# Optimization experiments

Hardware: AMD Instinct MI355X
Metric: run time of the kernel (lower is better)

The kernel has to match this reference:

```python
import jax, jax.numpy as jnp
import numpy as np

INPUT_DIM = 512
QUERY_DIM = 512
NUM_HEAD = 8
HEAD_DIM = INPUT_DIM // NUM_HEAD
SQRT_INPUT_DIM = INPUT_DIM ** 0.5
ELU_CLIP = 15.0  # elu_clip: elu followed by clamp to [-15, 15] (keeps exp finite)


def elu_clip(x):
    return jnp.clip(jax.nn.elu(x), -ELU_CLIP, ELU_CLIP)


def setup_inputs() -> dict:
    key = jax.random.key(0)
    k1, k2, k3, k4, k5, k6, k7 = jax.random.split(key, 7)
    B, S, Q = 8, 4096, 32
    inputs = jax.random.normal(k1, (B, S, INPUT_DIM), dtype=jnp.float32)
    queries = jax.random.normal(k2, (B, Q, QUERY_DIM), dtype=jnp.float32)
    masks = (jax.random.uniform(k3, (B, S)) > 0.1).astype(jnp.float32)
    # torch Linear params: weight [out, in], bias [out]
    lim_kv = 1.0 / np.sqrt(INPUT_DIM)
    Wkv = jax.random.uniform(k4, (2 * INPUT_DIM, INPUT_DIM), minval=-lim_kv, maxval=lim_kv, dtype=jnp.float32)
    bkv = jax.random.uniform(k5, (2 * INPUT_DIM,), minval=-lim_kv, maxval=lim_kv, dtype=jnp.float32)
    lim_q = 1.0 / np.sqrt(QUERY_DIM)
    Wq = jax.random.uniform(k6, (INPUT_DIM, QUERY_DIM), minval=-lim_q, maxval=lim_q, dtype=jnp.float32)
    bq = jax.random.uniform(k7, (INPUT_DIM,), minval=-lim_q, maxval=lim_q, dtype=jnp.float32)
    return {"inputs": inputs, "queries": queries, "masks": masks,
            "Wkv": Wkv, "bkv": bkv, "Wq": Wq, "bq": bq}


def reference(inputs, queries, masks, Wkv, bkv, Wq, bq):
    B, S, _ = inputs.shape
    Q = queries.shape[1]
    # k, v projections: [B,S,2I] -> [B,S,2,H,D]; index 0 along dim 2 is k, 1 is v
    kv = (inputs @ Wkv.T + bkv).reshape(B, S, 2, NUM_HEAD, HEAD_DIM)
    k, v = kv[:, :, 0], kv[:, :, 1]          # [B,S,H,D]
    q = (queries @ Wq.T + bq).reshape(B, Q, NUM_HEAD, HEAD_DIM)  # [B,Q,H,D]
    # scores: broadcast dot-product per head -> [B,Q,S,H]
    u = jnp.einsum('bqhd,bshd->bqsh', q, k)
    exp_u = jnp.exp(elu_clip(u / SQRT_INPUT_DIM))
    exp_u = exp_u * masks[:, None, :, None]
    attention = exp_u / jnp.sum(exp_u, axis=2, keepdims=True)
    # weighted sum over sequence -> [B,Q,H,D] -> [B,Q,I]
    attend = jnp.einsum('bqsh,bshd->bqhd', attention, v).reshape(B, Q, INPUT_DIM)
    return attend
```

## Files before the change

kernel.cpp:

```cpp
#include <hip/hip_runtime.h>
#include <hip/hip_bf16.h>


typedef float f32x4 __attribute__((ext_vector_type(4)));
typedef short s16x8 __attribute__((ext_vector_type(8)));

__device__ __forceinline__ unsigned short f2bf(float f) {
  union { __hip_bfloat16 h; unsigned short u; } cv;
  cv.h = __float2bfloat16(f);
  return cv.u;
}
__device__ __forceinline__ float bf2f(unsigned short u) {
  union { unsigned short u; __hip_bfloat16 h; } cv;
  cv.u = u;
  return __bfloat162float(cv.h);
}
__device__ __forceinline__ float tofl(float v) { return v; }
__device__ __forceinline__ float tofl(__hip_bfloat16 v) { return __bfloat162float(v); }

__device__ __forceinline__ f32x4 mfma16(s16x8 a, s16x8 b, f32x4 c) {
  return __builtin_amdgcn_mfma_f32_16x16x32_bf16(a, b, c, 0, 0, 0);
}

__device__ __forceinline__ int detect_fp32(const unsigned short* __restrict__ in16) {
  unsigned short v = in16[2 * (threadIdx.x & 63)];
  int e = (v >> 7) & 0xFF;
  unsigned long long m = __ballot(e >= 100 && e <= 130);
  return __popcll(m) < 48 ? 1 : 0;
}

__device__ __forceinline__ void gload_lds16(const void* g, void* s) {
  __builtin_amdgcn_global_load_lds(
      (const __attribute__((address_space(1))) unsigned int*)(g),
      (__attribute__((address_space(3))) unsigned int*)(s), 16, 0, 0);
}

__device__ __forceinline__ unsigned short* stg(unsigned short* buf, int r, int u) {
  return buf + r * 64 + ((u ^ (r & 7)) << 3);
}
__device__ __forceinline__ const unsigned short* stgc(const unsigned short* buf, int r, int u) {
  return buf + r * 64 + ((u ^ (r & 7)) << 3);
}
__device__ __forceinline__ int sw_idx(int r, int c) {
  return r * 128 + ((((c >> 3) ^ (r & 7)) << 3) | (c & 7));
}

template <typename T>
__device__ __forceinline__ s16x8 load_frag8(const T* p);
template <>
__device__ __forceinline__ s16x8 load_frag8<float>(const float* p) {
  const float4* q = reinterpret_cast<const float4*>(p);
  float4 a = q[0], b = q[1];
  union { unsigned short u[8]; s16x8 w; } t;
  t.u[0] = f2bf(a.x); t.u[1] = f2bf(a.y); t.u[2] = f2bf(a.z); t.u[3] = f2bf(a.w);
  t.u[4] = f2bf(b.x); t.u[5] = f2bf(b.y); t.u[6] = f2bf(b.z); t.u[7] = f2bf(b.w);
  return t.w;
}
template <>
__device__ __forceinline__ s16x8 load_frag8<__hip_bfloat16>(const __hip_bfloat16* p) {
  return *reinterpret_cast<const s16x8*>(p);
}

template <typename T> struct RegChunk;
template <> struct RegChunk<float> {
  float4 v[4];
  __device__ __forceinline__ void load(const float* p) {
    const float4* q = reinterpret_cast<const float4*>(p);
    v[0] = q[0]; v[1] = q[1]; v[2] = q[2]; v[3] = q[3];
  }
  __device__ __forceinline__ void store(unsigned short* d) {
    union { unsigned short u[16]; s16x8 w[2]; } t;
    const float* f = reinterpret_cast<const float*>(v);
#pragma unroll
    for (int i = 0; i < 16; ++i) t.u[i] = f2bf(f[i]);
    reinterpret_cast<s16x8*>(d)[0] = t.w[0];
    reinterpret_cast<s16x8*>(d)[1] = t.w[1];
  }
  __device__ __forceinline__ void store2(unsigned short* d0, unsigned short* d1) {
    union { unsigned short u[16]; s16x8 w[2]; } t;
    const float* f = reinterpret_cast<const float*>(v);
#pragma unroll
    for (int i = 0; i < 16; ++i) t.u[i] = f2bf(f[i]);
    *reinterpret_cast<s16x8*>(d0) = t.w[0];
    *reinterpret_cast<s16x8*>(d1) = t.w[1];
  }
};
template <> struct RegChunk<__hip_bfloat16> {
  s16x8 v[2];
  __device__ __forceinline__ void load(const __hip_bfloat16* p) {
    const s16x8* q = reinterpret_cast<const s16x8*>(p);
    v[0] = q[0]; v[1] = q[1];
  }
  __device__ __forceinline__ void store(unsigned short* d) {
    reinterpret_cast<s16x8*>(d)[0] = v[0];
    reinterpret_cast<s16x8*>(d)[1] = v[1];
  }
  __device__ __forceinline__ void store2(unsigned short* d0, unsigned short* d1) {
    *reinterpret_cast<s16x8*>(d0) = v[0];
    *reinterpret_cast<s16x8*>(d1) = v[1];
  }
};


#define CINP 0
#define CQ   16777216
#define CWKV 16908288
#define CWQ  17432576
#define CBKV 17694720
#define CBQ  17695744
#define CTOT 17696256

__global__ __launch_bounds__(256) void k_conv(const void* inputs, const void* queries,
                                              const void* Wkv, const void* Wq,
                                              const void* bkv, const void* bq,
                                              unsigned short* __restrict__ dst) {
  const int fp32 = detect_fp32((const unsigned short*)inputs);
  if (!fp32) return;
  const int bid = blockIdx.x, tid = threadIdx.x;
  if (bid < 2048) {
    size_t u = (size_t)bid * 1024 + tid;
#pragma unroll
    for (int k = 0; k < 4; ++k, u += 256) {
      size_t e = u * 8;
      s16x8 v = load_frag8<float>((const float*)inputs + e);
      *reinterpret_cast<s16x8*>(dst + e) = v;
    }
  } else {
    size_t i8 = (size_t)(bid - 2048) * 256 + tid;
    for (; i8 < 114880; i8 += (size_t)72 * 256) {
      size_t e = CQ + i8 * 8;
      const void* src;
      size_t off;
      if (e < CWKV) { src = queries; off = e - CQ; }
      else if (e < CWQ) { src = Wkv; off = e - CWKV; }
      else if (e < CBKV) { src = Wq; off = e - CWQ; }
      else if (e < CBQ) { src = bkv; off = e - CBKV; }
      else { src = bq; off = e - CBQ; }
      s16x8 v = load_frag8<float>((const float*)src + off);
      *reinterpret_cast<s16x8*>(dst + e) = v;
    }
  }
}

__global__ __launch_bounds__(256) void k_gemm2(const unsigned short* __restrict__ c,
                                               const void* inputs, const void* queries,
                                               const void* Wkv, const void* Wq,
                                               const void* bkv, const void* bq,
                                               unsigned short* __restrict__ kv,
                                               unsigned short* __restrict__ qws) {
  __shared__ unsigned short Ab[128 * 64];
  __shared__ unsigned short Bb[128 * 64];

  const int fp32 = detect_fp32((const unsigned short*)inputs);

  const int bid = blockIdx.x;
  const int t = (bid & 7) * 257 + (bid >> 3);
  const unsigned short *A, *W, *bias;
  unsigned short* dst;
  int dstride, Mt, Nt;
  if (t < 2048) {
    if (fp32) { A = c + CINP; W = c + CWKV; bias = c + CBKV; }
    else {
      A = (const unsigned short*)inputs;
      W = (const unsigned short*)Wkv;
      bias = (const unsigned short*)bkv;
    }
    dst = kv; dstride = 1024; Mt = t >> 3; Nt = t & 7;
  } else {
    const int tq = t - 2048;
    if (fp32) { A = c + CQ; W = c + CWQ; bias = c + CBQ; }
    else {
      A = (const unsigned short*)queries;
      W = (const unsigned short*)Wq;
      bias = (const unsigned short*)bq;
    }
    dst = qws; dstride = 512; Mt = tq >> 2; Nt = tq & 3;
  }

  const int tid = threadIdx.x;
  const int w = tid >> 6, l = tid & 63;
  const int quad = l >> 4, l16 = l & 15;
  const int wr = (w >> 1) * 64, wc = (w & 1) * 64;

  const int lrow = l >> 3;
  const int gsw = (l & 7) ^ lrow;

  const f32x4 zero4 = {0.f, 0.f, 0.f, 0.f};
  f32x4 acc[4][4];
#pragma unroll
  for (int i = 0; i < 4; ++i)
#pragma unroll
    for (int j = 0; j < 4; ++j) acc[i][j] = zero4;

  const size_t arow0 = (size_t)(Mt * 128) * 512;
  const size_t brow0 = (size_t)(Nt * 128) * 512;

#pragma unroll
  for (int k0 = 0; k0 < 512; k0 += 64) {
    __syncthreads();
#pragma unroll
    for (int k = 0; k < 4; ++k) {
      const int row = w * 32 + k * 8 + lrow;
      const int srcc = k0 + gsw * 8;
      gload_lds16(A + arow0 + (size_t)row * 512 + srcc, Ab + (w * 32 + k * 8) * 64);
      gload_lds16(W + brow0 + (size_t)row * 512 + srcc, Bb + (w * 32 + k * 8) * 64);
    }
    __syncthreads();
#pragma unroll
    for (int kk2 = 0; kk2 < 2; ++kk2) {
      s16x8 af[4], bfr[4];
#pragma unroll
      for (int i = 0; i < 4; ++i)
        af[i] = *reinterpret_cast<const s16x8*>(stgc(Ab, wr + i * 16 + l16, kk2 * 4 + quad));
#pragma unroll
      for (int j = 0; j < 4; ++j)
        bfr[j] = *reinterpret_cast<const s16x8*>(stgc(Bb, wc + j * 16 + l16, kk2 * 4 + quad));
#pragma unroll
      for (int i = 0; i < 4; ++i)
#pragma unroll
        for (int j = 0; j < 4; ++j) acc[i][j] = mfma16(af[i], bfr[j], acc[i][j]);
    }
  }

#pragma unroll
  for (int j = 0; j < 4; ++j) {
    float bb = bf2f(bias[Nt * 128 + wc + j * 16 + l16]);
#pragma unroll
    for (int i = 0; i < 4; ++i)
#pragma unroll
      for (int rg = 0; rg < 4; ++rg) {
        int row = Mt * 128 + wr + i * 16 + quad * 4 + rg;
        int col = Nt * 128 + wc + j * 16 + l16;
        dst[(size_t)row * dstride + col] = f2bf(acc[i][j][rg] + bb);
      }
  }
}

template <typename T>
__device__ __forceinline__ void attn_body(const unsigned short* __restrict__ kv,
                                          const unsigned short* __restrict__ qws,
                                          const T* __restrict__ masks,
                                          float* __restrict__ num_part,
                                          float* __restrict__ den_part,
                                          unsigned short* kvb, unsigned short* vtb,
                                          unsigned short* Pb, float* denL) {
  const int stile = blockIdx.x, b = blockIdx.y;
  const int s0 = stile * 128;
  const int tid = threadIdx.x;
  const int w = tid >> 6, l = tid & 63;
  const int quad = l >> 4, l16 = l & 15;
  const int hh = w >> 2, mt = (w >> 1) & 1, sh = w & 1, dh = w & 1;
  const int sr2 = tid >> 2, c0 = (tid & 3) * 32;
  const int rp2 = (tid >> 3) * 2;
  const int cb = (tid & 7) * 16;
  const f32x4 zero4 = {0.f, 0.f, 0.f, 0.f};
  const float scale = 0.044194173824159216f;
  const int bstile = b * 32 + stile;

  const unsigned short* kbase = kv + ((size_t)(b * 4096 + s0 + sr2)) * 1024;
  const unsigned short* vbase0 = kv + ((size_t)(b * 4096 + s0 + rp2)) * 1024 + 512;
  const unsigned short* vbase1 = vbase0 + 1024;

  s16x8 kp0, kp1, kp2, kp3, va0, va1, vb0, vb1;
  auto loadKV = [&](int hpi) {
    const unsigned short* kr = kbase + hpi * 128 + c0;
    kp0 = *reinterpret_cast<const s16x8*>(kr);
    kp1 = *reinterpret_cast<const s16x8*>(kr + 8);
    kp2 = *reinterpret_cast<const s16x8*>(kr + 16);
    kp3 = *reinterpret_cast<const s16x8*>(kr + 24);
    const unsigned short* v0 = vbase0 + hpi * 128 + cb;
    const unsigned short* v1 = vbase1 + hpi * 128 + cb;
    va0 = *reinterpret_cast<const s16x8*>(v0);
    va1 = *reinterpret_cast<const s16x8*>(v0 + 8);
    vb0 = *reinterpret_cast<const s16x8*>(v1);
    vb1 = *reinterpret_cast<const s16x8*>(v1 + 8);
  };
  loadKV(0);

#pragma unroll
  for (int hpi = 0; hpi < 4; ++hpi) {
    *reinterpret_cast<s16x8*>(&kvb[sw_idx(sr2, c0)]) = kp0;
    *reinterpret_cast<s16x8*>(&kvb[sw_idx(sr2, c0 + 8)]) = kp1;
    *reinterpret_cast<s16x8*>(&kvb[sw_idx(sr2, c0 + 16)]) = kp2;
    *reinterpret_cast<s16x8*>(&kvb[sw_idx(sr2, c0 + 24)]) = kp3;
    {
      union { s16x8 w; unsigned short u[8]; } a0, a1, b0, b1;
      a0.w = va0; a1.w = va1; b0.w = vb0; b1.w = vb1;
#pragma unroll
      for (int e = 0; e < 8; ++e) {
        unsigned int p0 = (unsigned int)a0.u[e] | ((unsigned int)b0.u[e] << 16);
        *reinterpret_cast<unsigned int*>(&vtb[sw_idx(cb + e, rp2)]) = p0;
        unsigned int p1 = (unsigned int)a1.u[e] | ((unsigned int)b1.u[e] << 16);
        *reinterpret_cast<unsigned int*>(&vtb[sw_idx(cb + 8 + e, rp2)]) = p1;
      }
    }
    if (hpi < 3) loadKV(hpi + 1);
    __syncthreads();

    {
      f32x4 ua[4];
#pragma unroll
      for (int j = 0; j < 4; ++j) ua[j] = zero4;
#pragma unroll
      for (int kk = 0; kk < 2; ++kk) {
        s16x8 aq = *reinterpret_cast<const s16x8*>(
            &qws[((size_t)(b * 32 + mt * 16 + l16)) * 512 + hpi * 128 + hh * 64 + kk * 32 +
                 quad * 8]);
#pragma unroll
        for (int j = 0; j < 4; ++j) {
          s16x8 bk = *reinterpret_cast<const s16x8*>(
              &kvb[sw_idx(sh * 64 + j * 16 + l16, hh * 64 + kk * 32 + quad * 8)]);
          ua[j] = mfma16(aq, bk, ua[j]);
        }
      }
      float dsum[4] = {0.f, 0.f, 0.f, 0.f};
#pragma unroll
      for (int j = 0; j < 4; ++j) {
        int scol = sh * 64 + j * 16 + l16;
        float mask = tofl(masks[(size_t)b * 4096 + s0 + scol]);
#pragma unroll
        for (int rg = 0; rg < 4; ++rg) {
          int qrow = mt * 16 + quad * 4 + rg;
          float uv = ua[j][rg] * scale;
          float e = uv > 0.f ? uv : (__expf(uv) - 1.f);
          e = fminf(e, 15.f);
          float p = __expf(e) * mask;
          unsigned short pu = f2bf(p);
          Pb[sw_idx(hh * 32 + qrow, scol)] = pu;
          dsum[rg] += bf2f(pu);
        }
      }
#pragma unroll
      for (int rg = 0; rg < 4; ++rg) {
        float s = dsum[rg];
        s += __shfl_xor(s, 1);
        s += __shfl_xor(s, 2);
        s += __shfl_xor(s, 4);
        s += __shfl_xor(s, 8);
        if (l16 == 0) denL[sh * 64 + hh * 32 + mt * 16 + quad * 4 + rg] = s;
      }
    }
    __syncthreads();

    if (tid < 64) {
      int qrow = tid & 31, hd = tid >> 5;
      den_part[((size_t)bstile * 32 + qrow) * 8 + hpi * 2 + hd] =
          denL[hd * 32 + qrow] + denL[64 + hd * 32 + qrow];
    }

    {
      f32x4 na0 = zero4, na1 = zero4;
#pragma unroll
      for (int kk = 0; kk < 4; ++kk) {
        s16x8 ap = *reinterpret_cast<const s16x8*>(
            &Pb[sw_idx(hh * 32 + mt * 16 + l16, kk * 32 + quad * 8)]);
        s16x8 bv0 = *reinterpret_cast<const s16x8*>(
            &vtb[sw_idx(hh * 64 + dh * 32 + l16, kk * 32 + quad * 8)]);
        s16x8 bv1 = *reinterpret_cast<const s16x8*>(
            &vtb[sw_idx(hh * 64 + dh * 32 + 16 + l16, kk * 32 + quad * 8)]);
        na0 = mfma16(ap, bv0, na0);
        na1 = mfma16(ap, bv1, na1);
      }
#pragma unroll
      for (int rg = 0; rg < 4; ++rg) {
        int qrow = mt * 16 + quad * 4 + rg;
        size_t base = ((size_t)bstile * 32 + qrow) * 512 + (hpi * 2 + hh) * 64 + dh * 32;
        num_part[base + l16] = na0[rg];
        num_part[base + 16 + l16] = na1[rg];
      }
    }
    __syncthreads();
  }
}

__global__ __launch_bounds__(512) void k_attn(const unsigned short* __restrict__ kv,
                                              const unsigned short* __restrict__ qws,
                                              const void* masks, float* __restrict__ num_part,
                                              float* __restrict__ den_part,
                                              const unsigned short* __restrict__ det) {
  __shared__ unsigned short kvb[128 * 128];
  __shared__ unsigned short vtb[128 * 128];
  __shared__ unsigned short Pb[64 * 128];
  __shared__ float denL[128];
  if (detect_fp32(det))
    attn_body<float>(kv, qws, (const float*)masks, num_part, den_part, kvb, vtb, Pb, denL);
  else
    attn_body<__hip_bfloat16>(kv, qws, (const __hip_bfloat16*)masks, num_part, den_part,
                              kvb, vtb, Pb, denL);
}

__global__ __launch_bounds__(256) void k_final(const float* __restrict__ num_part,
                                               const float* __restrict__ den_part, void* out,
                                               const unsigned short* __restrict__ det) {
  int i = blockIdx.x * 256 + threadIdx.x;
  int b = i >> 14, qhd = i & 16383;
  int q = (i >> 9) & 31, h = (i >> 6) & 7;
  float sn = 0.f, sd = 0.f;
#pragma unroll 4
  for (int st = 0; st < 32; ++st) {
    sn += num_part[(((size_t)(b * 32 + st)) << 14) + qhd];
    sd += den_part[((size_t)(b * 32 + st) * 32 + q) * 8 + h];
  }
  float v = sn / sd;
  if (detect_fp32(det))
    ((float*)out)[i] = v;
  else
    ((__hip_bfloat16*)out)[i] = __float2bfloat16(v);
}

template <typename T>
__device__ __forceinline__ void qproj_body_fb(const T* __restrict__ queries,
                                              const T* __restrict__ Wq,
                                              const T* __restrict__ bq,
                                              unsigned short* __restrict__ qws,
                                              unsigned short* Abuf, unsigned short* Bbuf) {
  const int Mt = blockIdx.x, Nt = blockIdx.y;
  const int tid = threadIdx.x;
  const int w = tid >> 6, l = tid & 63;
  const int quad = l >> 4, l16 = l & 15;
  const int wr = (w >> 1) * 64, wc = (w & 1) * 64;
  const int r_st = tid >> 1;
  const int kk_st = (tid & 1) * 16;
  const T* Asrc = queries + ((size_t)(Mt * 128 + r_st)) * 512 + kk_st;
  const T* Bsrc = Wq + ((size_t)(Nt * 128 + r_st)) * 512 + kk_st;

  const f32x4 zero4 = {0.f, 0.f, 0.f, 0.f};
  f32x4 acc[4][4];
#pragma unroll
  for (int i = 0; i < 4; ++i)
#pragma unroll
    for (int j = 0; j < 4; ++j) acc[i][j] = zero4;

  RegChunk<T> ra, rb;
  ra.load(Asrc);
  rb.load(Bsrc);
  for (int k0 = 0; k0 < 512; k0 += 32) {
    __syncthreads();
    ra.store(&Abuf[r_st * 32 + kk_st]);
    rb.store(&Bbuf[r_st * 32 + kk_st]);
    if (k0 + 32 < 512) {
      ra.load(Asrc + k0 + 32);
      rb.load(Bsrc + k0 + 32);
    }
    __syncthreads();
    s16x8 af[4], bfr[4];
#pragma unroll
    for (int i = 0; i < 4; ++i)
      af[i] = *reinterpret_cast<const s16x8*>(&Abuf[(wr + i * 16 + l16) * 32 + quad * 8]);
#pragma unroll
    for (int j = 0; j < 4; ++j)
      bfr[j] = *reinterpret_cast<const s16x8*>(&Bbuf[(wc + j * 16 + l16) * 32 + quad * 8]);
#pragma unroll
    for (int i = 0; i < 4; ++i)
#pragma unroll
      for (int j = 0; j < 4; ++j) acc[i][j] = mfma16(af[i], bfr[j], acc[i][j]);
  }
#pragma unroll
  for (int j = 0; j < 4; ++j) {
    float bb = tofl(bq[Nt * 128 + wc + j * 16 + l16]);
#pragma unroll
    for (int i = 0; i < 4; ++i)
#pragma unroll
      for (int rg = 0; rg < 4; ++rg) {
        int row = Mt * 128 + wr + i * 16 + quad * 4 + rg;
        int col = Nt * 128 + wc + j * 16 + l16;
        qws[(size_t)row * 512 + col] = f2bf(acc[i][j][rg] + bb);
      }
  }
}

__global__ __launch_bounds__(256) void k_qproj_fb(const void* queries, const void* Wq,
                                                  const void* bq, unsigned short* qws,
                                                  const unsigned short* __restrict__ det) {
  __shared__ unsigned short Abuf[128 * 32];
  __shared__ unsigned short Bbuf[128 * 32];
  if (detect_fp32(det))
    qproj_body_fb<float>((const float*)queries, (const float*)Wq, (const float*)bq, qws,
                         Abuf, Bbuf);
  else
    qproj_body_fb<__hip_bfloat16>((const __hip_bfloat16*)queries,
                                  (const __hip_bfloat16*)Wq, (const __hip_bfloat16*)bq, qws,
                                  Abuf, Bbuf);
}

template <typename T>
__device__ __forceinline__ void fused_body_fb(
    const T* __restrict__ inputs, const T* __restrict__ masks, const T* __restrict__ Wkv,
    const T* __restrict__ bkv, const unsigned short* __restrict__ qws,
    float* __restrict__ num, float* __restrict__ den, unsigned short* Abuf,
    unsigned short* Bbuf, unsigned short* kvbuf, unsigned short* vbuf,
    unsigned short* Pbuf) {
  const int stile = blockIdx.x;
  const int b = blockIdx.y;
  const int hp = blockIdx.z;
  const int s0 = stile * 128;
  const int tid = threadIdx.x;
  const int w = tid >> 6;
  const int l = tid & 63;
  const int quad = l >> 4;
  const int l16 = l & 15;
  const int which = w >> 2;
  const int wr = ((w >> 1) & 1) * 64;
  const int wc = (w & 1) * 64;

  const f32x4 zero4 = {0.f, 0.f, 0.f, 0.f};
  f32x4 acc[4][4];
#pragma unroll
  for (int i = 0; i < 4; ++i)
#pragma unroll
    for (int j = 0; j < 4; ++j) acc[i][j] = zero4;

  const int sr = tid >> 2;
  const int sc = tid & 3;
  const T* Asrc = inputs + ((size_t)(b * 4096 + s0 + sr)) * 512 + sc * 16;
  const T* BKs = Wkv + ((size_t)(hp * 128 + sr)) * 512 + sc * 16;
  const T* BVs = Wkv + ((size_t)(512 + hp * 128 + sr)) * 512 + sc * 16;
  unsigned short* ad0 = stg(Abuf, sr, sc * 2);
  unsigned short* ad1 = stg(Abuf, sr, sc * 2 + 1);
  unsigned short* bk0 = stg(Bbuf, sr, sc * 2);
  unsigned short* bk1 = stg(Bbuf, sr, sc * 2 + 1);
  unsigned short* bv0 = stg(Bbuf, 128 + sr, sc * 2);
  unsigned short* bv1 = stg(Bbuf, 128 + sr, sc * 2 + 1);

  RegChunk<T> ra0, ra1, rbk, rbv;
  ra0.load(Asrc);
  ra1.load(Asrc + 64);
  rbk.load(BKs);
  rbv.load(BVs);

#pragma unroll
  for (int it2 = 0; it2 < 4; ++it2) {
#pragma unroll
    for (int ph = 0; ph < 2; ++ph) {
      const int it = it2 * 2 + ph;
      RegChunk<T>& ra = ph ? ra1 : ra0;
      __syncthreads();
      ra.store2(ad0, ad1);
      rbk.store2(bk0, bk1);
      rbv.store2(bv0, bv1);
      if (it < 6) ra.load(Asrc + (it + 2) * 64);
      if (it < 7) {
        rbk.load(BKs + (it + 1) * 64);
        rbv.load(BVs + (it + 1) * 64);
      }
      __syncthreads();
#pragma unroll
      for (int kk2 = 0; kk2 < 2; ++kk2) {
        s16x8 af[4], bfr[4];
#pragma unroll
        for (int i = 0; i < 4; ++i)
          af[i] = *reinterpret_cast<const s16x8*>(stgc(Abuf, wr + i * 16 + l16, kk2 * 4 + quad));
#pragma unroll
        for (int j = 0; j < 4; ++j)
          bfr[j] = *reinterpret_cast<const s16x8*>(
              stgc(Bbuf, which * 128 + wc + j * 16 + l16, kk2 * 4 + quad));
#pragma unroll
        for (int i = 0; i < 4; ++i)
#pragma unroll
          for (int j = 0; j < 4; ++j) acc[i][j] = mfma16(af[i], bfr[j], acc[i][j]);
      }
    }
  }

#pragma unroll
  for (int j = 0; j < 4; ++j) {
    float bb = tofl(bkv[which * 512 + hp * 128 + wc + j * 16 + l16]);
#pragma unroll
    for (int i = 0; i < 4; ++i)
#pragma unroll
      for (int rg = 0; rg < 4; ++rg) {
        int sl = wr + i * 16 + quad * 4 + rg;
        int c = wc + j * 16 + l16;
        unsigned short bv = f2bf(acc[i][j][rg] + bb);
        if (which == 0)
          kvbuf[sw_idx(sl, c)] = bv;
        else
          vbuf[sw_idx(c, sl)] = bv;
      }
  }
  __syncthreads();

  const int hh = w >> 2, mt = (w >> 1) & 1, sh = w & 1;
  {
    f32x4 ua[4];
#pragma unroll
    for (int j = 0; j < 4; ++j) ua[j] = zero4;
#pragma unroll
    for (int kk = 0; kk < 2; ++kk) {
      s16x8 aq = *reinterpret_cast<const s16x8*>(
          qws + ((size_t)(b * 32 + mt * 16 + l16)) * 512 + hp * 128 + hh * 64 + kk * 32 +
          quad * 8);
#pragma unroll
      for (int j = 0; j < 4; ++j) {
        s16x8 bk = *reinterpret_cast<const s16x8*>(
            &kvbuf[sw_idx(sh * 64 + j * 16 + l16, hh * 64 + kk * 32 + quad * 8)]);
        ua[j] = mfma16(aq, bk, ua[j]);
      }
    }
    const float scale = 0.044194173824159216f;
    float dsum[4] = {0.f, 0.f, 0.f, 0.f};
#pragma unroll
    for (int j = 0; j < 4; ++j) {
      int scol = sh * 64 + j * 16 + l16;
      float mask = tofl(masks[(size_t)b * 4096 + s0 + scol]);
#pragma unroll
      for (int rg = 0; rg < 4; ++rg) {
        int qrow = mt * 16 + quad * 4 + rg;
        float uv = ua[j][rg] * scale;
        float e = uv > 0.f ? uv : (__expf(uv) - 1.f);
        e = fminf(e, 15.f);
        float p = __expf(e) * mask;
        unsigned short pu = f2bf(p);
        Pbuf[sw_idx(hh * 32 + qrow, scol)] = pu;
        dsum[rg] += bf2f(pu);
      }
    }
#pragma unroll
    for (int rg = 0; rg < 4; ++rg) {
      float s = dsum[rg];
      s += __shfl_xor(s, 1);
      s += __shfl_xor(s, 2);
      s += __shfl_xor(s, 4);
      s += __shfl_xor(s, 8);
      if (l16 == 0) {
        int qrow = mt * 16 + quad * 4 + rg;
        atomicAdd(&den[((size_t)(b * 32 + qrow)) * 8 + hp * 2 + hh], s);
      }
    }
  }
  __syncthreads();

  {
    const int dh = w & 1;
    f32x4 na[2];
    na[0] = zero4;
    na[1] = zero4;
#pragma unroll
    for (int kk = 0; kk < 4; ++kk) {
      s16x8 ap = *reinterpret_cast<const s16x8*>(
          &Pbuf[sw_idx(hh * 32 + mt * 16 + l16, kk * 32 + quad * 8)]);
#pragma unroll
      for (int jj = 0; jj < 2; ++jj) {
        int j = dh * 2 + jj;
        s16x8 bv = *reinterpret_cast<const s16x8*>(
            &vbuf[sw_idx(hh * 64 + j * 16 + l16, kk * 32 + quad * 8)]);
        na[jj] = mfma16(ap, bv, na[jj]);
      }
    }
    const int h = hp * 2 + hh;
#pragma unroll
    for (int jj = 0; jj < 2; ++jj) {
      int d = (dh * 2 + jj) * 16 + l16;
#pragma unroll
      for (int rg = 0; rg < 4; ++rg) {
        int qrow = mt * 16 + quad * 4 + rg;
        atomicAdd(&num[(((size_t)(b * 32 + qrow)) * 8 + h) * 64 + d], na[jj][rg]);
      }
    }
  }
}

__global__ __launch_bounds__(512, 2) void k_fused_fb(const void* inputs, const void* masks,
                                                     const void* Wkv, const void* bkv,
                                                     const unsigned short* __restrict__ qws,
                                                     float* __restrict__ num,
                                                     float* __restrict__ den) {
  __shared__ unsigned short Abuf[128 * 64];
  __shared__ unsigned short Bbuf[256 * 64];
  __shared__ unsigned short kvbuf[128 * 128];
  __shared__ unsigned short vbuf[128 * 128];
  __shared__ unsigned short Pbuf[64 * 128];
  if (detect_fp32((const unsigned short*)inputs))
    fused_body_fb<float>((const float*)inputs, (const float*)masks, (const float*)Wkv,
                         (const float*)bkv, qws, num, den, Abuf, Bbuf, kvbuf, vbuf, Pbuf);
  else
    fused_body_fb<__hip_bfloat16>((const __hip_bfloat16*)inputs,
                                  (const __hip_bfloat16*)masks, (const __hip_bfloat16*)Wkv,
                                  (const __hip_bfloat16*)bkv, qws, num, den, Abuf, Bbuf,
                                  kvbuf, vbuf, Pbuf);
}

__global__ __launch_bounds__(256) void k_div_fb(const float* __restrict__ num,
                                                const float* __restrict__ den, void* out,
                                                const unsigned short* __restrict__ det) {
  int i = blockIdx.x * 256 + threadIdx.x;
  float v = num[i] / den[i >> 6];
  if (detect_fp32(det))
    ((float*)out)[i] = v;
  else
    ((__hip_bfloat16*)out)[i] = __float2bfloat16(v);
}

extern "C" void kernel_launch(void* const* d_in, const int* in_sizes, int n_in,
                              void* d_out, int out_size, void* d_ws, size_t ws_size,
                              hipStream_t stream) {
  char* ws = (char*)d_ws;
  if (ws_size >= 119802880) {
    unsigned short* conv = (unsigned short*)ws;
    unsigned short* kv = (unsigned short*)(ws + 35392512);
    unsigned short* qws = (unsigned short*)(ws + 102501376);
    float* num_part = (float*)(ws + 102763520);
    float* den_part = (float*)(ws + 119540736);

    k_conv<<<2120, 256, 0, stream>>>(d_in[0], d_in[1], d_in[3], d_in[5], d_in[4], d_in[6],
                                     conv);
    k_gemm2<<<2056, 256, 0, stream>>>(conv, d_in[0], d_in[1], d_in[3], d_in[5], d_in[4],
                                      d_in[6], kv, qws);
    k_attn<<<dim3(32, 8), 512, 0, stream>>>(kv, qws, d_in[2], num_part, den_part,
                                            (const unsigned short*)d_in[0]);
    k_final<<<512, 256, 0, stream>>>(num_part, den_part, d_out,
                                     (const unsigned short*)d_in[0]);
  } else if (ws_size >= 802816) {
    float* den = (float*)(ws + 1024);
    float* num = (float*)(ws + 16384);
    unsigned short* qws = (unsigned short*)(ws + 540672);

    hipMemsetAsync(d_ws, 0, 540672, stream);
    dim3 gq(2, 4);
    k_qproj_fb<<<gq, 256, 0, stream>>>(d_in[1], d_in[5], d_in[6], qws,
                                       (const unsigned short*)d_in[0]);
    dim3 g2(32, 8, 4);
    k_fused_fb<<<g2, 512, 0, stream>>>(d_in[0], d_in[2], d_in[3], d_in[4], qws, num, den);
    k_div_fb<<<512, 256, 0, stream>>>(num, den, d_out, (const unsigned short*)d_in[0]);
  }
}
```

Before: 186.0 us.

## Split attention head-pairs across grid z and atomically accumulate denominators

The attention kernel's grid gains a z dimension of 2, and each block handles two head-pairs instead of four. This doubles the block count from 256 so the device's compute units are better filled. The shared-memory denominator staging is replaced by per-wave atomicAdd into den_part, which needs a memset before launch. Launch bounds now request 4 blocks per CU. The price is extra atomics, a memset, and some K/V rows being loaded by more blocks.

```diff
diff --git a/kernel.cpp b/kernel.cpp
--- a/kernel.cpp
+++ b/kernel.cpp
@@ -243,8 +243,9 @@
                                           float* __restrict__ num_part,
                                           float* __restrict__ den_part,
                                           unsigned short* kvb, unsigned short* vtb,
-                                          unsigned short* Pb, float* denL) {
+                                          unsigned short* Pb) {
   const int stile = blockIdx.x, b = blockIdx.y;
+  const int hp0 = blockIdx.z * 2;
   const int s0 = stile * 128;
   const int tid = threadIdx.x;
   const int w = tid >> 6, l = tid & 63;
@@ -275,10 +276,11 @@
     vb0 = *reinterpret_cast<const s16x8*>(v1);
     vb1 = *reinterpret_cast<const s16x8*>(v1 + 8);
   };
-  loadKV(0);
-
-#pragma unroll
-  for (int hpi = 0; hpi < 4; ++hpi) {
+  loadKV(hp0);
+
+#pragma unroll
+  for (int hi = 0; hi < 2; ++hi) {
+    const int hpi = hp0 + hi;
     *reinterpret_cast<s16x8*>(&kvb[sw_idx(sr2, c0)]) = kp0;
     *reinterpret_cast<s16x8*>(&kvb[sw_idx(sr2, c0 + 8)]) = kp1;
     *reinterpret_cast<s16x8*>(&kvb[sw_idx(sr2, c0 + 16)]) = kp2;
@@ -294,7 +296,7 @@
         *reinterpret_cast<unsigned int*>(&vtb[sw_idx(cb + 8 + e, rp2)]) = p1;
       }
     }
-    if (hpi < 3) loadKV(hpi + 1);
+    if (hi == 0) loadKV(hpi + 1);
     __syncthreads();
 
     {
@@ -337,16 +339,13 @@
         s += __shfl_xor(s, 2);
         s += __shfl_xor(s, 4);
         s += __shfl_xor(s, 8);
-        if (l16 == 0) denL[sh * 64 + hh * 32 + mt * 16 + quad * 4 + rg] = s;
+        if (l16 == 0) {
+          int qrow = mt * 16 + quad * 4 + rg;
+          atomicAdd(&den_part[((size_t)bstile * 32 + qrow) * 8 + hpi * 2 + hh], s);
+        }
       }
     }
     __syncthreads();
-
-    if (tid < 64) {
-      int qrow = tid & 31, hd = tid >> 5;
-      den_part[((size_t)bstile * 32 + qrow) * 8 + hpi * 2 + hd] =
-          denL[hd * 32 + qrow] + denL[64 + hd * 32 + qrow];
-    }
 
     {
       f32x4 na0 = zero4, na1 = zero4;
@@ -373,20 +372,20 @@
   }
 }
 
-__global__ __launch_bounds__(512) void k_attn(const unsigned short* __restrict__ kv,
-                                              const unsigned short* __restrict__ qws,
-                                              const void* masks, float* __restrict__ num_part,
-                                              float* __restrict__ den_part,
-                                              const unsigned short* __restrict__ det) {
+__global__ __launch_bounds__(512, 4) void k_attn(const unsigned short* __restrict__ kv,
+                                                 const unsigned short* __restrict__ qws,
+                                                 const void* masks,
+                                                 float* __restrict__ num_part,
+                                                 float* __restrict__ den_part,
+                                                 const unsigned short* __restrict__ det) {
   __shared__ unsigned short kvb[128 * 128];
   __shared__ unsigned short vtb[128 * 128];
   __shared__ unsigned short Pb[64 * 128];
-  __shared__ float denL[128];
   if (detect_fp32(det))
-    attn_body<float>(kv, qws, (const float*)masks, num_part, den_part, kvb, vtb, Pb, denL);
+    attn_body<float>(kv, qws, (const float*)masks, num_part, den_part, kvb, vtb, Pb);
   else
     attn_body<__hip_bfloat16>(kv, qws, (const __hip_bfloat16*)masks, num_part, den_part,
-                              kvb, vtb, Pb, denL);
+                              kvb, vtb, Pb);
 }
 
 __global__ __launch_bounds__(256) void k_final(const float* __restrict__ num_part,
@@ -702,12 +701,13 @@
     float* num_part = (float*)(ws + 102763520);
     float* den_part = (float*)(ws + 119540736);
 
+    hipMemsetAsync(den_part, 0, 262144, stream);
     k_conv<<<2120, 256, 0, stream>>>(d_in[0], d_in[1], d_in[3], d_in[5], d_in[4], d_in[6],
                                      conv);
     k_gemm2<<<2056, 256, 0, stream>>>(conv, d_in[0], d_in[1], d_in[3], d_in[5], d_in[4],
                                       d_in[6], kv, qws);
-    k_attn<<<dim3(32, 8), 512, 0, stream>>>(kv, qws, d_in[2], num_part, den_part,
-                                            (const unsigned short*)d_in[0]);
+    k_attn<<<dim3(32, 8, 2), 512, 0, stream>>>(kv, qws, d_in[2], num_part, den_part,
+                                               (const unsigned short*)d_in[0]);
     k_final<<<512, 256, 0, stream>>>(num_part, den_part, d_out,
                                      (const unsigned short*)d_in[0]);
   } else if (ws_size >= 802816) {
```

New measurement: 188.8 us. No clear change (+1.5%).
